# Kernel optimization log

Measured on AMD Instinct MI355X. Metric: run time of the kernel, lower is better.

Reference implementation:

```python
import jax, jax.numpy as jnp
import numpy as np

HIDDEN = 1024
MOE_FF = 512
SHARED_FF = 2816
NUM_EXPERTS = 16
TOP_K = 2
NORM_TOPK = True


def setup_inputs() -> dict:
    key = jax.random.key(0)
    ks = jax.random.split(key, 8)
    s = 0.02
    return {
        "layer_input": jax.random.normal(ks[0], (1, 2048, HIDDEN), dtype=jnp.float32),
        "gate_w": jax.random.normal(ks[1], (NUM_EXPERTS, HIDDEN), dtype=jnp.float32) * s,
        # fused gate_up weight per expert, laid out for x @ W: [E, hidden, 2*moe_ff]
        "w_gate_up": jax.random.normal(ks[2], (NUM_EXPERTS, HIDDEN, 2 * MOE_FF), dtype=jnp.float32) * s,
        # down weight per expert, laid out for h @ W: [E, moe_ff, hidden]
        "w_down": jax.random.normal(ks[3], (NUM_EXPERTS, MOE_FF, HIDDEN), dtype=jnp.float32) * s,
        # shared expert (Qwen2MoeMLP): Linear weights stored torch-style [out, in]
        "shared_w_gate": jax.random.normal(ks[4], (SHARED_FF, HIDDEN), dtype=jnp.float32) * s,
        "shared_w_up": jax.random.normal(ks[5], (SHARED_FF, HIDDEN), dtype=jnp.float32) * s,
        "shared_w_down": jax.random.normal(ks[6], (HIDDEN, SHARED_FF), dtype=jnp.float32) * s,
        "shared_gate_w": jax.random.normal(ks[7], (1, HIDDEN), dtype=jnp.float32) * s,
    }


def reference(layer_input, gate_w, w_gate_up, w_down,
              shared_w_gate, shared_w_up, shared_w_down, shared_gate_w):
    B, S, D = layer_input.shape
    x = layer_input.reshape(-1, D)  # [N, D]
    N = x.shape[0]

    # shared expert: silu-gated MLP, scaled by per-token sigmoid gate
    shared = (jax.nn.silu(x @ shared_w_gate.T) * (x @ shared_w_up.T)) @ shared_w_down.T
    shared = shared * jax.nn.sigmoid(x @ shared_gate_w.T)  # [N, D]

    # router: softmax in float32, top-k, optional renorm
    logits = x @ gate_w.T  # [N, E]
    probs = jax.nn.softmax(logits.astype(jnp.float32), axis=-1)
    rw, sel = jax.lax.top_k(probs, TOP_K)  # [N, K]
    if NORM_TOPK:
        rw = rw / rw.sum(axis=-1, keepdims=True)
    rw = rw.astype(x.dtype)

    # dense combine weights: zero for unselected experts (equivalent to
    # the sort/dispatch + grouped-GEMM + weighted scatter-combine)
    combine = jnp.zeros((N, NUM_EXPERTS), x.dtype).at[jnp.arange(N)[:, None], sel].set(rw)

    # expert gate_up projection, SwiGLU, down projection, weighted combine
    gu = jnp.einsum('nd,edf->nef', x, w_gate_up)  # [N, E, 2*moe_ff]
    g, h = jnp.split(gu, 2, axis=-1)
    h = jax.nn.silu(g) * h  # [N, E, moe_ff]
    expert_out = jnp.einsum('nef,efd,ne->nd', h, w_down, combine)  # [N, D]

    out = expert_out + shared
    return out.reshape(B, S, D)
```

## Files before the change

kernel.cpp:

```cpp
#include <hip/hip_runtime.h>
#include <hip/hip_bf16.h>

typedef unsigned short ushort_t;
typedef __bf16 bf16x8 __attribute__((ext_vector_type(8)));
typedef float f32x4 __attribute__((ext_vector_type(4)));

#define N_TOK 2048
#define DH    1024
#define FF    512
#define SFF   2816
#define NE    16

#define BM 128
#define BN 64
#define BK 64
#define LDK 72

__device__ __forceinline__ ushort_t f2bf(float f) {
  unsigned int x = __float_as_uint(f);
  unsigned int lsb = (x >> 16) & 1u;
  x += 0x7fffu + lsb;
  return (ushort_t)(x >> 16);
}
__device__ __forceinline__ float bf2f(ushort_t u) {
  union { unsigned int i; float f; } v; v.i = ((unsigned int)u) << 16; return v.f;
}
__device__ __forceinline__ uint4 cvt8v(const float4 a, const float4 b) {
  union { ushort_t u[8]; uint4 v; } r;
  r.u[0] = f2bf(a.x); r.u[1] = f2bf(a.y); r.u[2] = f2bf(a.z); r.u[3] = f2bf(a.w);
  r.u[4] = f2bf(b.x); r.u[5] = f2bf(b.y); r.u[6] = f2bf(b.z); r.u[7] = f2bf(b.w);
  return r.v;
}
__device__ __forceinline__ uint4 ld_cvt8(const float* __restrict__ p) {
  float4 a = *(const float4*)p;
  float4 b = *(const float4*)(p + 4);
  return cvt8v(a, b);
}

__global__ void router_kernel(const float* __restrict__ X, const float* __restrict__ GW,
                              const float* __restrict__ SGW,
                              int* __restrict__ sel, float* __restrict__ wtk,
                              float* __restrict__ sgate) {
  int wave = threadIdx.x >> 6, lane = threadIdx.x & 63;
  int n = blockIdx.x * 4 + wave;
  const float* x = X + (size_t)n * DH;
  int e = lane & 15, s = lane >> 4;
  const float* gw = GW + (size_t)e * DH;
  float lg = 0.f;
  for (int i = 0; i < 256; ++i) {
    int d = s * 256 + i;
    lg += x[d] * gw[d];
  }
  lg += __shfl_down(lg, 32);
  lg += __shfl_down(lg, 16);

  float gd = 0.f;
  #pragma unroll
  for (int i = 0; i < 16; ++i) {
    int d = lane * 16 + i;
    gd += x[d] * SGW[d];
  }
  #pragma unroll
  for (int off = 32; off >= 1; off >>= 1) gd += __shfl_down(gd, off);

  float l[16];
  #pragma unroll
  for (int i = 0; i < 16; ++i) l[i] = __shfl(lg, i);

  if (lane == 0) {
    int i1 = 0; float v1 = l[0];
    #pragma unroll
    for (int i = 1; i < 16; ++i) if (l[i] > v1) { v1 = l[i]; i1 = i; }
    int i2 = -1; float v2 = -1e30f;
    #pragma unroll
    for (int i = 0; i < 16; ++i) { if (i == i1) continue; if (l[i] > v2) { v2 = l[i]; i2 = i; } }
    float p2 = __expf(v2 - v1);
    float inv = 1.f / (1.f + p2);
    sel[n * 2 + 0] = i1; sel[n * 2 + 1] = i2;
    wtk[n * 2 + 0] = inv; wtk[n * 2 + 1] = p2 * inv;
    sgate[n] = 1.f / (1.f + __expf(-gd));
  }
}

__global__ void scatter_kernel(const int* __restrict__ sel,
                               int* __restrict__ toks, int* __restrict__ slot_of,
                               int* __restrict__ offs) {
  __shared__ int cnt[NE], bas[NE];
  int t = threadIdx.x;
  if (t < NE) cnt[t] = 0;
  __syncthreads();
  for (int i = t; i < N_TOK * 2; i += 256) atomicAdd(&cnt[sel[i]], 1);
  __syncthreads();
  if (t == 0) {
    int s = 0;
    for (int e = 0; e < NE; ++e) { bas[e] = s; offs[e] = s; s += cnt[e]; }
    offs[NE] = s;
  }
  __syncthreads();
  if (t < NE) cnt[t] = 0;
  __syncthreads();
  for (int i = t; i < N_TOK * 2; i += 256) {
    int e = sel[i];
    int p = atomicAdd(&cnt[e], 1);
    int slot = bas[e] + p;
    toks[slot] = i >> 1;
    slot_of[i] = slot;
  }
}

__global__ __launch_bounds__(256, 3) void gateup_kernel(
    const float* __restrict__ X, const float* __restrict__ WGU,
    const float* __restrict__ SWG, const float* __restrict__ SWU,
    ushort_t* __restrict__ HX, ushort_t* __restrict__ HS,
    const int* __restrict__ toks, const int* __restrict__ offs) {
  __shared__ __align__(16) ushort_t As[BM][LDK];
  __shared__ __align__(16) ushort_t Bgs[BN][LDK];
  __shared__ __align__(16) ushort_t Bus[BN][LDK];
  const int K = DH, NT = K / BK;

  int bid = blockIdx.x;
  int t = threadIdx.x;
  int wave = t >> 6, lane = t & 63;
  int wm = wave & 1, wn = wave >> 1;
  int qd = lane >> 4, l16 = lane & 15;
  int sr = t >> 3, sc = (t & 7) * 8;

  f32x4 accg[4][2], accu[4][2];
  #pragma unroll
  for (int i = 0; i < 4; ++i)
    #pragma unroll
    for (int j = 0; j < 2; ++j) {
      accg[i][j] = (f32x4){0.f, 0.f, 0.f, 0.f};
      accu[i][j] = (f32x4){0.f, 0.f, 0.f, 0.f};
    }

  int m0, n0, M, base, is_exp;

  if (bid < 704) {
    is_exp = 0; base = 0; M = N_TOK;
    n0 = (bid % 44) * BN; m0 = (bid / 44) * BM;
    const float* arow[4];
    const float *bgrow[2], *burow[2];
    #pragma unroll
    for (int p = 0; p < 4; ++p)
      arow[p] = X + (size_t)(m0 + sr + 32 * p) * K + sc;
    #pragma unroll
    for (int p = 0; p < 2; ++p) {
      bgrow[p] = SWG + (size_t)(n0 + sr + 32 * p) * K + sc;
      burow[p] = SWU + (size_t)(n0 + sr + 32 * p) * K + sc;
    }
    uint4 ar[4], bgr[2], bur[2];
    #pragma unroll
    for (int p = 0; p < 4; ++p) ar[p] = ld_cvt8(arow[p]);
    #pragma unroll
    for (int p = 0; p < 2; ++p) { bgr[p] = ld_cvt8(bgrow[p]); bur[p] = ld_cvt8(burow[p]); }

    for (int kt = 0; kt < NT; ++kt) {
      #pragma unroll
      for (int p = 0; p < 4; ++p)
        *(uint4*)&As[sr + 32 * p][sc] = ar[p];
      #pragma unroll
      for (int p = 0; p < 2; ++p) {
        *(uint4*)&Bgs[sr + 32 * p][sc] = bgr[p];
        *(uint4*)&Bus[sr + 32 * p][sc] = bur[p];
      }
      __syncthreads();
      if (kt + 1 < NT) {
        int ko = (kt + 1) * BK;
        #pragma unroll
        for (int p = 0; p < 4; ++p) ar[p] = ld_cvt8(arow[p] + ko);
        #pragma unroll
        for (int p = 0; p < 2; ++p) { bgr[p] = ld_cvt8(bgrow[p] + ko); bur[p] = ld_cvt8(burow[p] + ko); }
      }
      #pragma unroll
      for (int ks = 0; ks < 2; ++ks) {
        int kk = ks * 32 + qd * 8;
        bf16x8 af[4], bgf[2], buf[2];
        #pragma unroll
        for (int i = 0; i < 4; ++i)
          af[i] = *(const bf16x8*)&As[wm * 64 + i * 16 + l16][kk];
        #pragma unroll
        for (int j = 0; j < 2; ++j) {
          bgf[j] = *(const bf16x8*)&Bgs[wn * 32 + j * 16 + l16][kk];
          buf[j] = *(const bf16x8*)&Bus[wn * 32 + j * 16 + l16][kk];
        }
        #pragma unroll
        for (int i = 0; i < 4; ++i)
          #pragma unroll
          for (int j = 0; j < 2; ++j) {
            accg[i][j] = __builtin_amdgcn_mfma_f32_16x16x32_bf16(af[i], bgf[j], accg[i][j], 0, 0, 0);
            accu[i][j] = __builtin_amdgcn_mfma_f32_16x16x32_bf16(af[i], buf[j], accu[i][j], 0, 0, 0);
          }
      }
      __syncthreads();
    }
  } else {
    is_exp = 1;
    int b2 = bid - 704;
    int e = b2 >> 7, rem = b2 & 127;
    n0 = (rem & 7) * BN; m0 = (rem >> 3) * BM;
    base = offs[e]; M = offs[e + 1] - base;
    if (m0 >= M) return;
    const float* W = WGU + (size_t)e * DH * (2 * FF);
    int tn = t & 63, tk = (t >> 6) * 16;

    const float* arow[4];
    #pragma unroll
    for (int p = 0; p < 4; ++p) {
      int m = m0 + sr + 32 * p;
      int mm = m < M ? m : (M - 1);
      arow[p] = X + (size_t)toks[base + mm] * K + sc;
    }
    const float* wkb = W + (size_t)tk * (2 * FF) + n0 + tn;

    uint4 ar[4];
    float bgr[16], bur[16];
    #pragma unroll
    for (int p = 0; p < 4; ++p) ar[p] = ld_cvt8(arow[p]);
    #pragma unroll
    for (int j = 0; j < 16; ++j) {
      bgr[j] = wkb[(size_t)j * (2 * FF)];
      bur[j] = wkb[(size_t)j * (2 * FF) + FF];
    }

    for (int kt = 0; kt < NT; ++kt) {
      #pragma unroll
      for (int p = 0; p < 4; ++p)
        *(uint4*)&As[sr + 32 * p][sc] = ar[p];
      {
        union { ushort_t u[8]; uint4 v; } g0, g1, u0, u1;
        #pragma unroll
        for (int j = 0; j < 8; ++j) {
          g0.u[j] = f2bf(bgr[j]); g1.u[j] = f2bf(bgr[8 + j]);
          u0.u[j] = f2bf(bur[j]); u1.u[j] = f2bf(bur[8 + j]);
        }
        *(uint4*)&Bgs[tn][tk]     = g0.v;
        *(uint4*)&Bgs[tn][tk + 8] = g1.v;
        *(uint4*)&Bus[tn][tk]     = u0.v;
        *(uint4*)&Bus[tn][tk + 8] = u1.v;
      }
      __syncthreads();
      if (kt + 1 < NT) {
        int ko = (kt + 1) * BK;
        #pragma unroll
        for (int p = 0; p < 4; ++p) ar[p] = ld_cvt8(arow[p] + ko);
        const float* wk = wkb + (size_t)ko * (2 * FF);
        #pragma unroll
        for (int j = 0; j < 16; ++j) {
          bgr[j] = wk[(size_t)j * (2 * FF)];
          bur[j] = wk[(size_t)j * (2 * FF) + FF];
        }
      }
      #pragma unroll
      for (int ks = 0; ks < 2; ++ks) {
        int kk = ks * 32 + qd * 8;
        bf16x8 af[4], bgf[2], buf[2];
        #pragma unroll
        for (int i = 0; i < 4; ++i)
          af[i] = *(const bf16x8*)&As[wm * 64 + i * 16 + l16][kk];
        #pragma unroll
        for (int j = 0; j < 2; ++j) {
          bgf[j] = *(const bf16x8*)&Bgs[wn * 32 + j * 16 + l16][kk];
          buf[j] = *(const bf16x8*)&Bus[wn * 32 + j * 16 + l16][kk];
        }
        #pragma unroll
        for (int i = 0; i < 4; ++i)
          #pragma unroll
          for (int j = 0; j < 2; ++j) {
            accg[i][j] = __builtin_amdgcn_mfma_f32_16x16x32_bf16(af[i], bgf[j], accg[i][j], 0, 0, 0);
            accu[i][j] = __builtin_amdgcn_mfma_f32_16x16x32_bf16(af[i], buf[j], accu[i][j], 0, 0, 0);
          }
      }
      __syncthreads();
    }
  }

  #pragma unroll
  for (int i = 0; i < 4; ++i)
    #pragma unroll
    for (int r = 0; r < 4; ++r) {
      int row = wm * 64 + i * 16 + qd * 4 + r;
      #pragma unroll
      for (int j = 0; j < 2; ++j) {
        float g = accg[i][j][r], u = accu[i][j][r];
        float h = g / (1.f + __expf(-g)) * u;
        As[row][wn * 32 + j * 16 + l16] = f2bf(h);
      }
    }
  __syncthreads();
  if (is_exp) {
    #pragma unroll
    for (int p = 0; p < 4; ++p) {
      int m = m0 + sr + 32 * p;
      if (m < M)
        *(uint4*)(HX + (size_t)(base + m) * FF + n0 + sc) = *(uint4*)&As[sr + 32 * p][sc];
    }
  } else {
    #pragma unroll
    for (int p = 0; p < 4; ++p) {
      int m = m0 + sr + 32 * p;
      *(uint4*)(HS + (size_t)m * SFF + n0 + sc) = *(uint4*)&As[sr + 32 * p][sc];
    }
  }
}

__global__ __launch_bounds__(256, 4) void down_kernel(
    const ushort_t* __restrict__ HX, const ushort_t* __restrict__ HS,
    const float* __restrict__ WDN, const float* __restrict__ SWD,
    ushort_t* __restrict__ SD0, ushort_t* __restrict__ SD1,
    ushort_t* __restrict__ EXPO, const int* __restrict__ offs) {
  __shared__ __align__(16) ushort_t As[BM][LDK];
  __shared__ __align__(16) ushort_t Bs[BN][LDK];

  int bid = blockIdx.x;
  int t = threadIdx.x;
  int wave = t >> 6, lane = t & 63;
  int wm = wave & 1, wn = wave >> 1;
  int qd = lane >> 4, l16 = lane & 15;
  int sr = t >> 3, sc = (t & 7) * 8;

  f32x4 c[4][2];
  #pragma unroll
  for (int i = 0; i < 4; ++i)
    #pragma unroll
    for (int j = 0; j < 2; ++j) c[i][j] = (f32x4){0.f, 0.f, 0.f, 0.f};

  int m0, n0, M, base_row;
  ushort_t* outp;

  if (bid < 512) {
    int kz = bid >> 8, rem = bid & 255;
    m0 = (rem >> 4) * BM; n0 = (rem & 15) * BN;
    M = N_TOK; base_row = 0;
    const int KC = SFF / 2, NT = KC / BK;
    int kb = kz * KC;
    outp = kz ? SD1 : SD0;

    const ushort_t* arow[4];
    const float* brow[2];
    #pragma unroll
    for (int p = 0; p < 4; ++p)
      arow[p] = HS + (size_t)(m0 + sr + 32 * p) * SFF + kb + sc;
    #pragma unroll
    for (int p = 0; p < 2; ++p)
      brow[p] = SWD + (size_t)(n0 + sr + 32 * p) * SFF + kb + sc;

    uint4 ar[4], br[2];
    #pragma unroll
    for (int p = 0; p < 4; ++p) ar[p] = *(const uint4*)(arow[p]);
    #pragma unroll
    for (int p = 0; p < 2; ++p) br[p] = ld_cvt8(brow[p]);

    for (int kt = 0; kt < NT; ++kt) {
      #pragma unroll
      for (int p = 0; p < 4; ++p)
        *(uint4*)&As[sr + 32 * p][sc] = ar[p];
      #pragma unroll
      for (int p = 0; p < 2; ++p)
        *(uint4*)&Bs[sr + 32 * p][sc] = br[p];
      __syncthreads();
      if (kt + 1 < NT) {
        int ko = (kt + 1) * BK;
        #pragma unroll
        for (int p = 0; p < 4; ++p) ar[p] = *(const uint4*)(arow[p] + ko);
        #pragma unroll
        for (int p = 0; p < 2; ++p) br[p] = ld_cvt8(brow[p] + ko);
      }
      #pragma unroll
      for (int ks = 0; ks < 2; ++ks) {
        int kk = ks * 32 + qd * 8;
        bf16x8 af[4], bf[2];
        #pragma unroll
        for (int i = 0; i < 4; ++i)
          af[i] = *(const bf16x8*)&As[wm * 64 + i * 16 + l16][kk];
        #pragma unroll
        for (int j = 0; j < 2; ++j)
          bf[j] = *(const bf16x8*)&Bs[wn * 32 + j * 16 + l16][kk];
        #pragma unroll
        for (int i = 0; i < 4; ++i)
          #pragma unroll
          for (int j = 0; j < 2; ++j)
            c[i][j] = __builtin_amdgcn_mfma_f32_16x16x32_bf16(af[i], bf[j], c[i][j], 0, 0, 0);
      }
      __syncthreads();
    }
  } else {
    int b2 = bid - 512;
    int e = b2 >> 8, rem = b2 & 255;
    n0 = (rem & 15) * BN; m0 = (rem >> 4) * BM;
    int base = offs[e];
    M = offs[e + 1] - base;
    if (m0 >= M) return;
    base_row = base;
    const int NT = FF / BK;
    const float* W = WDN + (size_t)e * FF * DH;
    const ushort_t* A = HX + (size_t)base * FF;
    int tn = t & 63, tk = (t >> 6) * 16;
    outp = EXPO;

    const ushort_t* arow[4];
    #pragma unroll
    for (int p = 0; p < 4; ++p) {
      int m = m0 + sr + 32 * p;
      int mm = m < M ? m : (M - 1);
      arow[p] = A + (size_t)mm * FF + sc;
    }
    const float* wkb = W + (size_t)tk * DH + n0 + tn;

    uint4 ar[4];
    float br[16];
    #pragma unroll
    for (int p = 0; p < 4; ++p) ar[p] = *(const uint4*)(arow[p]);
    #pragma unroll
    for (int j = 0; j < 16; ++j) br[j] = wkb[(size_t)j * DH];

    for (int kt = 0; kt < NT; ++kt) {
      #pragma unroll
      for (int p = 0; p < 4; ++p)
        *(uint4*)&As[sr + 32 * p][sc] = ar[p];
      {
        union { ushort_t u[8]; uint4 v; } b0, b1;
        #pragma unroll
        for (int j = 0; j < 8; ++j) { b0.u[j] = f2bf(br[j]); b1.u[j] = f2bf(br[8 + j]); }
        *(uint4*)&Bs[tn][tk]     = b0.v;
        *(uint4*)&Bs[tn][tk + 8] = b1.v;
      }
      __syncthreads();
      if (kt + 1 < NT) {
        int ko = (kt + 1) * BK;
        #pragma unroll
        for (int p = 0; p < 4; ++p) ar[p] = *(const uint4*)(arow[p] + ko);
        const float* wk = wkb + (size_t)ko * DH;
        #pragma unroll
        for (int j = 0; j < 16; ++j) br[j] = wk[(size_t)j * DH];
      }
      #pragma unroll
      for (int ks = 0; ks < 2; ++ks) {
        int kk = ks * 32 + qd * 8;
        bf16x8 af[4], bf[2];
        #pragma unroll
        for (int i = 0; i < 4; ++i)
          af[i] = *(const bf16x8*)&As[wm * 64 + i * 16 + l16][kk];
        #pragma unroll
        for (int j = 0; j < 2; ++j)
          bf[j] = *(const bf16x8*)&Bs[wn * 32 + j * 16 + l16][kk];
        #pragma unroll
        for (int i = 0; i < 4; ++i)
          #pragma unroll
          for (int j = 0; j < 2; ++j)
            c[i][j] = __builtin_amdgcn_mfma_f32_16x16x32_bf16(af[i], bf[j], c[i][j], 0, 0, 0);
      }
      __syncthreads();
    }
  }

  #pragma unroll
  for (int i = 0; i < 4; ++i)
    #pragma unroll
    for (int r = 0; r < 4; ++r) {
      int row = wm * 64 + i * 16 + qd * 4 + r;
      #pragma unroll
      for (int j = 0; j < 2; ++j)
        As[row][wn * 32 + j * 16 + l16] = f2bf(c[i][j][r]);
    }
  __syncthreads();
  #pragma unroll
  for (int p = 0; p < 4; ++p) {
    int m = m0 + sr + 32 * p;
    if (m < M)
      *(uint4*)(outp + (size_t)(base_row + m) * DH + n0 + sc) = *(uint4*)&As[sr + 32 * p][sc];
  }
}

__global__ void combine_kernel(const ushort_t* __restrict__ SD0, const ushort_t* __restrict__ SD1,
                               const ushort_t* __restrict__ EXPO,
                               const float* __restrict__ sgate, const float* __restrict__ wtk,
                               const int* __restrict__ slot_of, float* __restrict__ out) {
  int n = blockIdx.x, t = threadIdx.x;
  float sg = sgate[n];
  float w0 = wtk[n * 2 + 0], w1 = wtk[n * 2 + 1];
  int s0 = slot_of[n * 2 + 0], s1 = slot_of[n * 2 + 1];
  int col = t * 4;
  ushort4 d0 = *(const ushort4*)(SD0 + (size_t)n * DH + col);
  ushort4 d1 = *(const ushort4*)(SD1 + (size_t)n * DH + col);
  ushort4 a  = *(const ushort4*)(EXPO + (size_t)s0 * DH + col);
  ushort4 b  = *(const ushort4*)(EXPO + (size_t)s1 * DH + col);
  float4 o;
  o.x = sg * (bf2f(d0.x) + bf2f(d1.x)) + w0 * bf2f(a.x) + w1 * bf2f(b.x);
  o.y = sg * (bf2f(d0.y) + bf2f(d1.y)) + w0 * bf2f(a.y) + w1 * bf2f(b.y);
  o.z = sg * (bf2f(d0.z) + bf2f(d1.z)) + w0 * bf2f(a.z) + w1 * bf2f(b.z);
  o.w = sg * (bf2f(d0.w) + bf2f(d1.w)) + w0 * bf2f(a.w) + w1 * bf2f(b.w);
  *(float4*)(out + (size_t)n * DH + col) = o;
}

extern "C" void kernel_launch(void* const* d_in, const int* in_sizes, int n_in,
                              void* d_out, int out_size, void* d_ws, size_t ws_size,
                              hipStream_t stream) {
  const float* x    = (const float*)d_in[0];
  const float* gw   = (const float*)d_in[1];
  const float* wgu  = (const float*)d_in[2];
  const float* wdn  = (const float*)d_in[3];
  const float* swg  = (const float*)d_in[4];
  const float* swu  = (const float*)d_in[5];
  const float* swd  = (const float*)d_in[6];
  const float* sgw  = (const float*)d_in[7];
  float* out = (float*)d_out;

  char* ws = (char*)d_ws;
  constexpr size_t OFF_HS   = 0;
  constexpr size_t OFF_HX   = OFF_HS   + (size_t)N_TOK * SFF * 2;
  constexpr size_t OFF_SD0  = OFF_HX   + (size_t)4096 * FF * 2;
  constexpr size_t OFF_SD1  = OFF_SD0  + (size_t)N_TOK * DH * 2;
  constexpr size_t OFF_EXPO = OFF_SD1  + (size_t)N_TOK * DH * 2;
  constexpr size_t OFF_TOK  = OFF_EXPO + (size_t)4096 * DH * 2;
  constexpr size_t OFF_OFFS = OFF_TOK  + 4096 * 4;
  constexpr size_t OFF_SEL  = OFF_OFFS + 32 * 4;
  constexpr size_t OFF_WTK  = OFF_SEL  + 4096 * 4;
  constexpr size_t OFF_SG   = OFF_WTK  + 4096 * 4;
  constexpr size_t OFF_SLOT = OFF_SG   + 2048 * 4;

  ushort_t* hs    = (ushort_t*)(ws + OFF_HS);
  ushort_t* hx    = (ushort_t*)(ws + OFF_HX);
  ushort_t* sd0   = (ushort_t*)(ws + OFF_SD0);
  ushort_t* sd1   = (ushort_t*)(ws + OFF_SD1);
  ushort_t* expo  = (ushort_t*)(ws + OFF_EXPO);
  int*      toks  = (int*)(ws + OFF_TOK);
  int*      offs  = (int*)(ws + OFF_OFFS);
  int*      sel   = (int*)(ws + OFF_SEL);
  float*    wtk   = (float*)(ws + OFF_WTK);
  float*    sgate = (float*)(ws + OFF_SG);
  int*      slot_of = (int*)(ws + OFF_SLOT);

  router_kernel<<<N_TOK / 4, 256, 0, stream>>>(x, gw, sgw, sel, wtk, sgate);
  scatter_kernel<<<1, 256, 0, stream>>>(sel, toks, slot_of, offs);
  gateup_kernel<<<704 + 2048, 256, 0, stream>>>(x, wgu, swg, swu, hx, hs, toks, offs);
  down_kernel<<<512 + 4096, 256, 0, stream>>>(hx, hs, wdn, swd, sd0, sd1, expo, offs);
  combine_kernel<<<N_TOK, 256, 0, stream>>>(sd0, sd1, expo, sgate, wtk, slot_of, out);
}
```

Baseline: 409.4 us.

## Pre-convert activations and shared weights to bf16 in a separate kernel

Adds a convert kernel that casts the input activations and the three shared-expert weight matrices from fp32 to bf16 once per call. The gate-up and down GEMMs then load bf16 directly instead of loading fp32 and converting per tile. This halves the global traffic inside those GEMMs and drops the repeated conversion work, at the cost of an extra kernel that reads all the fp32 data and writes the bf16 copies. It also switches f2bf to the native __bf16 cast and raises the launch-bounds occupancy hints on both GEMM kernels.

```diff
diff --git a/kernel.cpp b/kernel.cpp
--- a/kernel.cpp
+++ b/kernel.cpp
@@ -17,10 +17,8 @@
 #define LDK 72
 
 __device__ __forceinline__ ushort_t f2bf(float f) {
-  unsigned int x = __float_as_uint(f);
-  unsigned int lsb = (x >> 16) & 1u;
-  x += 0x7fffu + lsb;
-  return (ushort_t)(x >> 16);
+  __bf16 h = (__bf16)f;
+  union { __bf16 h; ushort_t u; } v; v.h = h; return v.u;
 }
 __device__ __forceinline__ float bf2f(ushort_t u) {
   union { unsigned int i; float f; } v; v.i = ((unsigned int)u) << 16; return v.f;
@@ -35,6 +33,21 @@
   float4 a = *(const float4*)p;
   float4 b = *(const float4*)(p + 4);
   return cvt8v(a, b);
+}
+
+__global__ void convert_kernel(const float* __restrict__ X, const float* __restrict__ SWG,
+                               const float* __restrict__ SWU, const float* __restrict__ SWD,
+                               ushort_t* __restrict__ XB, ushort_t* __restrict__ SWGB,
+                               ushort_t* __restrict__ SWUB, ushort_t* __restrict__ SWDB) {
+  const int NX = N_TOK * DH / 8;
+  const int NS = SFF * DH / 8;
+  int i = blockIdx.x * 256 + threadIdx.x;
+  const float* s; ushort_t* d; int off;
+  if (i < NX)               { s = X;   d = XB;   off = i; }
+  else if (i < NX + NS)     { s = SWG; d = SWGB; off = i - NX; }
+  else if (i < NX + 2 * NS) { s = SWU; d = SWUB; off = i - NX - NS; }
+  else                      { s = SWD; d = SWDB; off = i - NX - 2 * NS; }
+  *(uint4*)(d + (size_t)off * 8) = ld_cvt8(s + (size_t)off * 8);
 }
 
 __global__ void router_kernel(const float* __restrict__ X, const float* __restrict__ GW,
@@ -108,9 +121,9 @@
   }
 }
 
-__global__ __launch_bounds__(256, 3) void gateup_kernel(
-    const float* __restrict__ X, const float* __restrict__ WGU,
-    const float* __restrict__ SWG, const float* __restrict__ SWU,
+__global__ __launch_bounds__(256, 4) void gateup_kernel(
+    const ushort_t* __restrict__ XB, const float* __restrict__ WGU,
+    const ushort_t* __restrict__ SWGB, const ushort_t* __restrict__ SWUB,
     ushort_t* __restrict__ HX, ushort_t* __restrict__ HS,
     const int* __restrict__ toks, const int* __restrict__ offs) {
   __shared__ __align__(16) ushort_t As[BM][LDK];
@@ -139,21 +152,21 @@
   if (bid < 704) {
     is_exp = 0; base = 0; M = N_TOK;
     n0 = (bid % 44) * BN; m0 = (bid / 44) * BM;
-    const float* arow[4];
-    const float *bgrow[2], *burow[2];
+    const ushort_t* arow[4];
+    const ushort_t *bgrow[2], *burow[2];
     #pragma unroll
     for (int p = 0; p < 4; ++p)
-      arow[p] = X + (size_t)(m0 + sr + 32 * p) * K + sc;
+      arow[p] = XB + (size_t)(m0 + sr + 32 * p) * K + sc;
     #pragma unroll
     for (int p = 0; p < 2; ++p) {
-      bgrow[p] = SWG + (size_t)(n0 + sr + 32 * p) * K + sc;
-      burow[p] = SWU + (size_t)(n0 + sr + 32 * p) * K + sc;
+      bgrow[p] = SWGB + (size_t)(n0 + sr + 32 * p) * K + sc;
+      burow[p] = SWUB + (size_t)(n0 + sr + 32 * p) * K + sc;
     }
     uint4 ar[4], bgr[2], bur[2];
     #pragma unroll
-    for (int p = 0; p < 4; ++p) ar[p] = ld_cvt8(arow[p]);
-    #pragma unroll
-    for (int p = 0; p < 2; ++p) { bgr[p] = ld_cvt8(bgrow[p]); bur[p] = ld_cvt8(burow[p]); }
+    for (int p = 0; p < 4; ++p) ar[p] = *(const uint4*)arow[p];
+    #pragma unroll
+    for (int p = 0; p < 2; ++p) { bgr[p] = *(const uint4*)bgrow[p]; bur[p] = *(const uint4*)burow[p]; }
 
     for (int kt = 0; kt < NT; ++kt) {
       #pragma unroll
@@ -168,9 +181,9 @@
       if (kt + 1 < NT) {
         int ko = (kt + 1) * BK;
         #pragma unroll
-        for (int p = 0; p < 4; ++p) ar[p] = ld_cvt8(arow[p] + ko);
-        #pragma unroll
-        for (int p = 0; p < 2; ++p) { bgr[p] = ld_cvt8(bgrow[p] + ko); bur[p] = ld_cvt8(burow[p] + ko); }
+        for (int p = 0; p < 4; ++p) ar[p] = *(const uint4*)(arow[p] + ko);
+        #pragma unroll
+        for (int p = 0; p < 2; ++p) { bgr[p] = *(const uint4*)(bgrow[p] + ko); bur[p] = *(const uint4*)(burow[p] + ko); }
       }
       #pragma unroll
       for (int ks = 0; ks < 2; ++ks) {
@@ -204,19 +217,19 @@
     const float* W = WGU + (size_t)e * DH * (2 * FF);
     int tn = t & 63, tk = (t >> 6) * 16;
 
-    const float* arow[4];
+    const ushort_t* arow[4];
     #pragma unroll
     for (int p = 0; p < 4; ++p) {
       int m = m0 + sr + 32 * p;
       int mm = m < M ? m : (M - 1);
-      arow[p] = X + (size_t)toks[base + mm] * K + sc;
+      arow[p] = XB + (size_t)toks[base + mm] * K + sc;
     }
     const float* wkb = W + (size_t)tk * (2 * FF) + n0 + tn;
 
     uint4 ar[4];
     float bgr[16], bur[16];
     #pragma unroll
-    for (int p = 0; p < 4; ++p) ar[p] = ld_cvt8(arow[p]);
+    for (int p = 0; p < 4; ++p) ar[p] = *(const uint4*)arow[p];
     #pragma unroll
     for (int j = 0; j < 16; ++j) {
       bgr[j] = wkb[(size_t)j * (2 * FF)];
@@ -243,7 +256,7 @@
       if (kt + 1 < NT) {
         int ko = (kt + 1) * BK;
         #pragma unroll
-        for (int p = 0; p < 4; ++p) ar[p] = ld_cvt8(arow[p] + ko);
+        for (int p = 0; p < 4; ++p) ar[p] = *(const uint4*)(arow[p] + ko);
         const float* wk = wkb + (size_t)ko * (2 * FF);
         #pragma unroll
         for (int j = 0; j < 16; ++j) {
@@ -304,9 +317,9 @@
   }
 }
 
-__global__ __launch_bounds__(256, 4) void down_kernel(
+__global__ __launch_bounds__(256, 5) void down_kernel(
     const ushort_t* __restrict__ HX, const ushort_t* __restrict__ HS,
-    const float* __restrict__ WDN, const float* __restrict__ SWD,
+    const float* __restrict__ WDN, const ushort_t* __restrict__ SWDB,
     ushort_t* __restrict__ SD0, ushort_t* __restrict__ SD1,
     ushort_t* __restrict__ EXPO, const int* __restrict__ offs) {
   __shared__ __align__(16) ushort_t As[BM][LDK];
@@ -337,19 +350,19 @@
     outp = kz ? SD1 : SD0;
 
     const ushort_t* arow[4];
-    const float* brow[2];
+    const ushort_t* brow[2];
     #pragma unroll
     for (int p = 0; p < 4; ++p)
       arow[p] = HS + (size_t)(m0 + sr + 32 * p) * SFF + kb + sc;
     #pragma unroll
     for (int p = 0; p < 2; ++p)
-      brow[p] = SWD + (size_t)(n0 + sr + 32 * p) * SFF + kb + sc;
+      brow[p] = SWDB + (size_t)(n0 + sr + 32 * p) * SFF + kb + sc;
 
     uint4 ar[4], br[2];
     #pragma unroll
     for (int p = 0; p < 4; ++p) ar[p] = *(const uint4*)(arow[p]);
     #pragma unroll
-    for (int p = 0; p < 2; ++p) br[p] = ld_cvt8(brow[p]);
+    for (int p = 0; p < 2; ++p) br[p] = *(const uint4*)(brow[p]);
 
     for (int kt = 0; kt < NT; ++kt) {
       #pragma unroll
@@ -364,7 +377,7 @@
         #pragma unroll
         for (int p = 0; p < 4; ++p) ar[p] = *(const uint4*)(arow[p] + ko);
         #pragma unroll
-        for (int p = 0; p < 2; ++p) br[p] = ld_cvt8(brow[p] + ko);
+        for (int p = 0; p < 2; ++p) br[p] = *(const uint4*)(brow[p] + ko);
       }
       #pragma unroll
       for (int ks = 0; ks < 2; ++ks) {
@@ -512,7 +525,11 @@
   constexpr size_t OFF_SD0  = OFF_HX   + (size_t)4096 * FF * 2;
   constexpr size_t OFF_SD1  = OFF_SD0  + (size_t)N_TOK * DH * 2;
   constexpr size_t OFF_EXPO = OFF_SD1  + (size_t)N_TOK * DH * 2;
-  constexpr size_t OFF_TOK  = OFF_EXPO + (size_t)4096 * DH * 2;
+  constexpr size_t OFF_XB   = OFF_EXPO + (size_t)4096 * DH * 2;
+  constexpr size_t OFF_SWGB = OFF_XB   + (size_t)N_TOK * DH * 2;
+  constexpr size_t OFF_SWUB = OFF_SWGB + (size_t)SFF * DH * 2;
+  constexpr size_t OFF_SWDB = OFF_SWUB + (size_t)SFF * DH * 2;
+  constexpr size_t OFF_TOK  = OFF_SWDB + (size_t)SFF * DH * 2;
   constexpr size_t OFF_OFFS = OFF_TOK  + 4096 * 4;
   constexpr size_t OFF_SEL  = OFF_OFFS + 32 * 4;
   constexpr size_t OFF_WTK  = OFF_SEL  + 4096 * 4;
@@ -524,6 +541,10 @@
   ushort_t* sd0   = (ushort_t*)(ws + OFF_SD0);
   ushort_t* sd1   = (ushort_t*)(ws + OFF_SD1);
   ushort_t* expo  = (ushort_t*)(ws + OFF_EXPO);
+  ushort_t* xb    = (ushort_t*)(ws + OFF_XB);
+  ushort_t* swgb  = (ushort_t*)(ws + OFF_SWGB);
+  ushort_t* swub  = (ushort_t*)(ws + OFF_SWUB);
+  ushort_t* swdb  = (ushort_t*)(ws + OFF_SWDB);
   int*      toks  = (int*)(ws + OFF_TOK);
   int*      offs  = (int*)(ws + OFF_OFFS);
   int*      sel   = (int*)(ws + OFF_SEL);
@@ -531,9 +552,10 @@
   float*    sgate = (float*)(ws + OFF_SG);
   int*      slot_of = (int*)(ws + OFF_SLOT);
 
+  convert_kernel<<<5248, 256, 0, stream>>>(x, swg, swu, swd, xb, swgb, swub, swdb);
   router_kernel<<<N_TOK / 4, 256, 0, stream>>>(x, gw, sgw, sel, wtk, sgate);
   scatter_kernel<<<1, 256, 0, stream>>>(sel, toks, slot_of, offs);
-  gateup_kernel<<<704 + 2048, 256, 0, stream>>>(x, wgu, swg, swu, hx, hs, toks, offs);
-  down_kernel<<<512 + 4096, 256, 0, stream>>>(hx, hs, wdn, swd, sd0, sd1, expo, offs);
+  gateup_kernel<<<704 + 2048, 256, 0, stream>>>(xb, wgu, swgb, swub, hx, hs, toks, offs);
+  down_kernel<<<512 + 4096, 256, 0, stream>>>(hx, hs, wdn, swdb, sd0, sd1, expo, offs);
   combine_kernel<<<N_TOK, 256, 0, stream>>>(sd0, sd1, expo, sgate, wtk, slot_of, out);
 }
```

After: 514.7 us. 25.7% more time.

## Pre-transpose and bf16-convert expert weights into K-contiguous workspace layout

Applied to the files above, without the earlier changes.

Adds a per-call kernel that transposes and converts the fp32 expert gate_up and down weights into bf16 [N][K] layout in workspace. The expert GEMM paths then load B tiles with 16-byte vector loads and store them straight into shared memory, with no per-element conversion. This replaces the old scattered strided scalar fp32 weight loads. The cost is an extra pass that reads all expert weights (about 96MB fp32) and writes them back as bf16, run on every call.

```diff
diff --git a/kernel.cpp b/kernel.cpp
--- a/kernel.cpp
+++ b/kernel.cpp
@@ -35,6 +35,39 @@
   float4 a = *(const float4*)p;
   float4 b = *(const float4*)(p + 4);
   return cvt8v(a, b);
+}
+
+__global__ void transpose_kernel(const float* __restrict__ WGU, const float* __restrict__ WDN,
+                                 ushort_t* __restrict__ WGUB, ushort_t* __restrict__ WDNB) {
+  __shared__ ushort_t tl[64][72];
+  int bid = blockIdx.x;
+  const float* src; ushort_t* dst; int K, N, kt, nt;
+  if (bid < 4096) {
+    int e = bid >> 8, rem = bid & 255; kt = rem >> 4; nt = rem & 15;
+    src = WGU + (size_t)e * DH * (2 * FF); dst = WGUB + (size_t)e * (2 * FF) * DH;
+    K = DH; N = 2 * FF;
+  } else {
+    int b2 = bid - 4096;
+    int e = b2 >> 7, rem = b2 & 127; kt = rem >> 4; nt = rem & 15;
+    src = WDN + (size_t)e * FF * DH; dst = WDNB + (size_t)e * DH * FF;
+    K = FF; N = DH;
+  }
+  int t = threadIdx.x;
+  int k0 = kt * 64, n0 = nt * 64;
+  int r = t >> 2, c0 = (t & 3) * 16;
+  const float* sp = src + (size_t)(k0 + r) * N + n0 + c0;
+  #pragma unroll
+  for (int q = 0; q < 4; ++q) {
+    float4 v = *(const float4*)(sp + q * 4);
+    tl[c0 + q * 4 + 0][r] = f2bf(v.x);
+    tl[c0 + q * 4 + 1][r] = f2bf(v.y);
+    tl[c0 + q * 4 + 2][r] = f2bf(v.z);
+    tl[c0 + q * 4 + 3][r] = f2bf(v.w);
+  }
+  __syncthreads();
+  ushort_t* dp = dst + (size_t)(n0 + r) * K + k0 + c0;
+  *(uint4*)(dp)     = *(uint4*)&tl[r][c0];
+  *(uint4*)(dp + 8) = *(uint4*)&tl[r][c0 + 8];
 }
 
 __global__ void router_kernel(const float* __restrict__ X, const float* __restrict__ GW,
@@ -109,7 +142,7 @@
 }
 
 __global__ __launch_bounds__(256, 3) void gateup_kernel(
-    const float* __restrict__ X, const float* __restrict__ WGU,
+    const float* __restrict__ X, const ushort_t* __restrict__ WGUB,
     const float* __restrict__ SWG, const float* __restrict__ SWU,
     ushort_t* __restrict__ HX, ushort_t* __restrict__ HS,
     const int* __restrict__ toks, const int* __restrict__ offs) {
@@ -201,8 +234,7 @@
     n0 = (rem & 7) * BN; m0 = (rem >> 3) * BM;
     base = offs[e]; M = offs[e + 1] - base;
     if (m0 >= M) return;
-    const float* W = WGU + (size_t)e * DH * (2 * FF);
-    int tn = t & 63, tk = (t >> 6) * 16;
+    const ushort_t* Wt = WGUB + (size_t)e * (2 * FF) * DH;
 
     const float* arow[4];
     #pragma unroll
@@ -211,45 +243,35 @@
       int mm = m < M ? m : (M - 1);
       arow[p] = X + (size_t)toks[base + mm] * K + sc;
     }
-    const float* wkb = W + (size_t)tk * (2 * FF) + n0 + tn;
-
-    uint4 ar[4];
-    float bgr[16], bur[16];
+    const ushort_t *bgrow[2], *burow[2];
+    #pragma unroll
+    for (int p = 0; p < 2; ++p) {
+      bgrow[p] = Wt + (size_t)(n0 + sr + 32 * p) * DH + sc;
+      burow[p] = Wt + (size_t)(FF + n0 + sr + 32 * p) * DH + sc;
+    }
+
+    uint4 ar[4], bgr[2], bur[2];
     #pragma unroll
     for (int p = 0; p < 4; ++p) ar[p] = ld_cvt8(arow[p]);
     #pragma unroll
-    for (int j = 0; j < 16; ++j) {
-      bgr[j] = wkb[(size_t)j * (2 * FF)];
-      bur[j] = wkb[(size_t)j * (2 * FF) + FF];
-    }
+    for (int p = 0; p < 2; ++p) { bgr[p] = *(const uint4*)bgrow[p]; bur[p] = *(const uint4*)burow[p]; }
 
     for (int kt = 0; kt < NT; ++kt) {
       #pragma unroll
       for (int p = 0; p < 4; ++p)
         *(uint4*)&As[sr + 32 * p][sc] = ar[p];
-      {
-        union { ushort_t u[8]; uint4 v; } g0, g1, u0, u1;
-        #pragma unroll
-        for (int j = 0; j < 8; ++j) {
-          g0.u[j] = f2bf(bgr[j]); g1.u[j] = f2bf(bgr[8 + j]);
-          u0.u[j] = f2bf(bur[j]); u1.u[j] = f2bf(bur[8 + j]);
-        }
-        *(uint4*)&Bgs[tn][tk]     = g0.v;
-        *(uint4*)&Bgs[tn][tk + 8] = g1.v;
-        *(uint4*)&Bus[tn][tk]     = u0.v;
-        *(uint4*)&Bus[tn][tk + 8] = u1.v;
+      #pragma unroll
+      for (int p = 0; p < 2; ++p) {
+        *(uint4*)&Bgs[sr + 32 * p][sc] = bgr[p];
+        *(uint4*)&Bus[sr + 32 * p][sc] = bur[p];
       }
       __syncthreads();
       if (kt + 1 < NT) {
         int ko = (kt + 1) * BK;
         #pragma unroll
         for (int p = 0; p < 4; ++p) ar[p] = ld_cvt8(arow[p] + ko);
-        const float* wk = wkb + (size_t)ko * (2 * FF);
-        #pragma unroll
-        for (int j = 0; j < 16; ++j) {
-          bgr[j] = wk[(size_t)j * (2 * FF)];
-          bur[j] = wk[(size_t)j * (2 * FF) + FF];
-        }
+        #pragma unroll
+        for (int p = 0; p < 2; ++p) { bgr[p] = *(const uint4*)(bgrow[p] + ko); bur[p] = *(const uint4*)(burow[p] + ko); }
       }
       #pragma unroll
       for (int ks = 0; ks < 2; ++ks) {
@@ -306,7 +328,7 @@
 
 __global__ __launch_bounds__(256, 4) void down_kernel(
     const ushort_t* __restrict__ HX, const ushort_t* __restrict__ HS,
-    const float* __restrict__ WDN, const float* __restrict__ SWD,
+    const ushort_t* __restrict__ WDNB, const float* __restrict__ SWD,
     ushort_t* __restrict__ SD0, ushort_t* __restrict__ SD1,
     ushort_t* __restrict__ EXPO, const int* __restrict__ offs) {
   __shared__ __align__(16) ushort_t As[BM][LDK];
@@ -393,9 +415,8 @@
     if (m0 >= M) return;
     base_row = base;
     const int NT = FF / BK;
-    const float* W = WDN + (size_t)e * FF * DH;
+    const ushort_t* Wd = WDNB + (size_t)e * DH * FF;
     const ushort_t* A = HX + (size_t)base * FF;
-    int tn = t & 63, tk = (t >> 6) * 16;
     outp = EXPO;
 
     const ushort_t* arow[4];
@@ -405,34 +426,31 @@
       int mm = m < M ? m : (M - 1);
       arow[p] = A + (size_t)mm * FF + sc;
     }
-    const float* wkb = W + (size_t)tk * DH + n0 + tn;
-
-    uint4 ar[4];
-    float br[16];
+    const ushort_t* brow[2];
+    #pragma unroll
+    for (int p = 0; p < 2; ++p)
+      brow[p] = Wd + (size_t)(n0 + sr + 32 * p) * FF + sc;
+
+    uint4 ar[4], br[2];
     #pragma unroll
     for (int p = 0; p < 4; ++p) ar[p] = *(const uint4*)(arow[p]);
     #pragma unroll
-    for (int j = 0; j < 16; ++j) br[j] = wkb[(size_t)j * DH];
+    for (int p = 0; p < 2; ++p) br[p] = *(const uint4*)(brow[p]);
 
     for (int kt = 0; kt < NT; ++kt) {
       #pragma unroll
       for (int p = 0; p < 4; ++p)
         *(uint4*)&As[sr + 32 * p][sc] = ar[p];
-      {
-        union { ushort_t u[8]; uint4 v; } b0, b1;
-        #pragma unroll
-        for (int j = 0; j < 8; ++j) { b0.u[j] = f2bf(br[j]); b1.u[j] = f2bf(br[8 + j]); }
-        *(uint4*)&Bs[tn][tk]     = b0.v;
-        *(uint4*)&Bs[tn][tk + 8] = b1.v;
-      }
+      #pragma unroll
+      for (int p = 0; p < 2; ++p)
+        *(uint4*)&Bs[sr + 32 * p][sc] = br[p];
       __syncthreads();
       if (kt + 1 < NT) {
         int ko = (kt + 1) * BK;
         #pragma unroll
         for (int p = 0; p < 4; ++p) ar[p] = *(const uint4*)(arow[p] + ko);
-        const float* wk = wkb + (size_t)ko * DH;
-        #pragma unroll
-        for (int j = 0; j < 16; ++j) br[j] = wk[(size_t)j * DH];
+        #pragma unroll
+        for (int p = 0; p < 2; ++p) br[p] = *(const uint4*)(brow[p] + ko);
       }
       #pragma unroll
       for (int ks = 0; ks < 2; ++ks) {
@@ -512,7 +530,9 @@
   constexpr size_t OFF_SD0  = OFF_HX   + (size_t)4096 * FF * 2;
   constexpr size_t OFF_SD1  = OFF_SD0  + (size_t)N_TOK * DH * 2;
   constexpr size_t OFF_EXPO = OFF_SD1  + (size_t)N_TOK * DH * 2;
-  constexpr size_t OFF_TOK  = OFF_EXPO + (size_t)4096 * DH * 2;
+  constexpr size_t OFF_WGUB = OFF_EXPO + (size_t)4096 * DH * 2;
+  constexpr size_t OFF_WDNB = OFF_WGUB + (size_t)NE * (2 * FF) * DH * 2;
+  constexpr size_t OFF_TOK  = OFF_WDNB + (size_t)NE * DH * FF * 2;
   constexpr size_t OFF_OFFS = OFF_TOK  + 4096 * 4;
   constexpr size_t OFF_SEL  = OFF_OFFS + 32 * 4;
   constexpr size_t OFF_WTK  = OFF_SEL  + 4096 * 4;
@@ -524,6 +544,8 @@
   ushort_t* sd0   = (ushort_t*)(ws + OFF_SD0);
   ushort_t* sd1   = (ushort_t*)(ws + OFF_SD1);
   ushort_t* expo  = (ushort_t*)(ws + OFF_EXPO);
+  ushort_t* wgub  = (ushort_t*)(ws + OFF_WGUB);
+  ushort_t* wdnb  = (ushort_t*)(ws + OFF_WDNB);
   int*      toks  = (int*)(ws + OFF_TOK);
   int*      offs  = (int*)(ws + OFF_OFFS);
   int*      sel   = (int*)(ws + OFF_SEL);
@@ -531,9 +553,10 @@
   float*    sgate = (float*)(ws + OFF_SG);
   int*      slot_of = (int*)(ws + OFF_SLOT);
 
+  transpose_kernel<<<4096 + 2048, 256, 0, stream>>>(wgu, wdn, wgub, wdnb);
   router_kernel<<<N_TOK / 4, 256, 0, stream>>>(x, gw, sgw, sel, wtk, sgate);
   scatter_kernel<<<1, 256, 0, stream>>>(sel, toks, slot_of, offs);
-  gateup_kernel<<<704 + 2048, 256, 0, stream>>>(x, wgu, swg, swu, hx, hs, toks, offs);
-  down_kernel<<<512 + 4096, 256, 0, stream>>>(hx, hs, wdn, swd, sd0, sd1, expo, offs);
+  gateup_kernel<<<704 + 2048, 256, 0, stream>>>(x, wgub, swg, swu, hx, hs, toks, offs);
+  down_kernel<<<512 + 4096, 256, 0, stream>>>(hx, hs, wdnb, swd, sd0, sd1, expo, offs);
   combine_kernel<<<N_TOK, 256, 0, stream>>>(sd0, sd1, expo, sgate, wtk, slot_of, out);
 }
```

After: 460.1 us. +12.4%, slower.

## Pre-transpose expert down weights to bf16 and vectorize router dot products

Applied to the files above, without the earlier changes.

Adds a kernel that converts the expert down-projection weights to bf16 and transposes them to [E, hidden, ff], so down_kernel can load B tiles with contiguous 16-byte reads instead of strided scalar fp32 loads followed by per-element conversion. The router's logit and shared-gate dot products also switch to float4 loads. The transpose runs on every call, costing an extra 32 MB fp32 read and 16 MB bf16 write, while the many down_kernel tiles that reread each expert's weights become cheaper.

```diff
diff --git a/kernel.cpp b/kernel.cpp
--- a/kernel.cpp
+++ b/kernel.cpp
@@ -35,6 +35,31 @@
   float4 a = *(const float4*)p;
   float4 b = *(const float4*)(p + 4);
   return cvt8v(a, b);
+}
+
+__global__ void transpose_kernel(const float* __restrict__ WDN, ushort_t* __restrict__ WDNB) {
+  __shared__ ushort_t tl[64][72];
+  int bid = blockIdx.x;
+  int e = bid >> 7, rem = bid & 127;
+  int kt = rem >> 4, nt = rem & 15;
+  const float* src = WDN + (size_t)e * FF * DH;
+  ushort_t* dst = WDNB + (size_t)e * DH * FF;
+  int t = threadIdx.x;
+  int k0 = kt * 64, n0 = nt * 64;
+  int r = t >> 2, c0 = (t & 3) * 16;
+  const float* sp = src + (size_t)(k0 + r) * DH + n0 + c0;
+  #pragma unroll
+  for (int q = 0; q < 4; ++q) {
+    float4 v = *(const float4*)(sp + q * 4);
+    tl[c0 + q * 4 + 0][r] = f2bf(v.x);
+    tl[c0 + q * 4 + 1][r] = f2bf(v.y);
+    tl[c0 + q * 4 + 2][r] = f2bf(v.z);
+    tl[c0 + q * 4 + 3][r] = f2bf(v.w);
+  }
+  __syncthreads();
+  ushort_t* dp = dst + (size_t)(n0 + r) * FF + k0 + c0;
+  *(uint4*)(dp)     = *(uint4*)&tl[r][c0];
+  *(uint4*)(dp + 8) = *(uint4*)&tl[r][c0 + 8];
 }
 
 __global__ void router_kernel(const float* __restrict__ X, const float* __restrict__ GW,
@@ -47,18 +72,23 @@
   int e = lane & 15, s = lane >> 4;
   const float* gw = GW + (size_t)e * DH;
   float lg = 0.f;
-  for (int i = 0; i < 256; ++i) {
-    int d = s * 256 + i;
-    lg += x[d] * gw[d];
+  #pragma unroll
+  for (int i = 0; i < 64; ++i) {
+    int d = s * 256 + i * 4;
+    float4 xv = *(const float4*)(x + d);
+    float4 gv = *(const float4*)(gw + d);
+    lg += xv.x * gv.x + xv.y * gv.y + xv.z * gv.z + xv.w * gv.w;
   }
   lg += __shfl_down(lg, 32);
   lg += __shfl_down(lg, 16);
 
   float gd = 0.f;
   #pragma unroll
-  for (int i = 0; i < 16; ++i) {
-    int d = lane * 16 + i;
-    gd += x[d] * SGW[d];
+  for (int i = 0; i < 4; ++i) {
+    int d = lane * 16 + i * 4;
+    float4 xv = *(const float4*)(x + d);
+    float4 gv = *(const float4*)(SGW + d);
+    gd += xv.x * gv.x + xv.y * gv.y + xv.z * gv.z + xv.w * gv.w;
   }
   #pragma unroll
   for (int off = 32; off >= 1; off >>= 1) gd += __shfl_down(gd, off);
@@ -306,7 +336,7 @@
 
 __global__ __launch_bounds__(256, 4) void down_kernel(
     const ushort_t* __restrict__ HX, const ushort_t* __restrict__ HS,
-    const float* __restrict__ WDN, const float* __restrict__ SWD,
+    const ushort_t* __restrict__ WDNB, const float* __restrict__ SWD,
     ushort_t* __restrict__ SD0, ushort_t* __restrict__ SD1,
     ushort_t* __restrict__ EXPO, const int* __restrict__ offs) {
   __shared__ __align__(16) ushort_t As[BM][LDK];
@@ -393,9 +423,8 @@
     if (m0 >= M) return;
     base_row = base;
     const int NT = FF / BK;
-    const float* W = WDN + (size_t)e * FF * DH;
+    const ushort_t* Wd = WDNB + (size_t)e * DH * FF;
     const ushort_t* A = HX + (size_t)base * FF;
-    int tn = t & 63, tk = (t >> 6) * 16;
     outp = EXPO;
 
     const ushort_t* arow[4];
@@ -405,34 +434,31 @@
       int mm = m < M ? m : (M - 1);
       arow[p] = A + (size_t)mm * FF + sc;
     }
-    const float* wkb = W + (size_t)tk * DH + n0 + tn;
-
-    uint4 ar[4];
-    float br[16];
+    const ushort_t* brow[2];
+    #pragma unroll
+    for (int p = 0; p < 2; ++p)
+      brow[p] = Wd + (size_t)(n0 + sr + 32 * p) * FF + sc;
+
+    uint4 ar[4], br[2];
     #pragma unroll
     for (int p = 0; p < 4; ++p) ar[p] = *(const uint4*)(arow[p]);
     #pragma unroll
-    for (int j = 0; j < 16; ++j) br[j] = wkb[(size_t)j * DH];
+    for (int p = 0; p < 2; ++p) br[p] = *(const uint4*)(brow[p]);
 
     for (int kt = 0; kt < NT; ++kt) {
       #pragma unroll
       for (int p = 0; p < 4; ++p)
         *(uint4*)&As[sr + 32 * p][sc] = ar[p];
-      {
-        union { ushort_t u[8]; uint4 v; } b0, b1;
-        #pragma unroll
-        for (int j = 0; j < 8; ++j) { b0.u[j] = f2bf(br[j]); b1.u[j] = f2bf(br[8 + j]); }
-        *(uint4*)&Bs[tn][tk]     = b0.v;
-        *(uint4*)&Bs[tn][tk + 8] = b1.v;
-      }
+      #pragma unroll
+      for (int p = 0; p < 2; ++p)
+        *(uint4*)&Bs[sr + 32 * p][sc] = br[p];
       __syncthreads();
       if (kt + 1 < NT) {
         int ko = (kt + 1) * BK;
         #pragma unroll
         for (int p = 0; p < 4; ++p) ar[p] = *(const uint4*)(arow[p] + ko);
-        const float* wk = wkb + (size_t)ko * DH;
-        #pragma unroll
-        for (int j = 0; j < 16; ++j) br[j] = wk[(size_t)j * DH];
+        #pragma unroll
+        for (int p = 0; p < 2; ++p) br[p] = *(const uint4*)(brow[p] + ko);
       }
       #pragma unroll
       for (int ks = 0; ks < 2; ++ks) {
@@ -512,7 +538,8 @@
   constexpr size_t OFF_SD0  = OFF_HX   + (size_t)4096 * FF * 2;
   constexpr size_t OFF_SD1  = OFF_SD0  + (size_t)N_TOK * DH * 2;
   constexpr size_t OFF_EXPO = OFF_SD1  + (size_t)N_TOK * DH * 2;
-  constexpr size_t OFF_TOK  = OFF_EXPO + (size_t)4096 * DH * 2;
+  constexpr size_t OFF_WDNB = OFF_EXPO + (size_t)4096 * DH * 2;
+  constexpr size_t OFF_TOK  = OFF_WDNB + (size_t)NE * DH * FF * 2;
   constexpr size_t OFF_OFFS = OFF_TOK  + 4096 * 4;
   constexpr size_t OFF_SEL  = OFF_OFFS + 32 * 4;
   constexpr size_t OFF_WTK  = OFF_SEL  + 4096 * 4;
@@ -524,6 +551,7 @@
   ushort_t* sd0   = (ushort_t*)(ws + OFF_SD0);
   ushort_t* sd1   = (ushort_t*)(ws + OFF_SD1);
   ushort_t* expo  = (ushort_t*)(ws + OFF_EXPO);
+  ushort_t* wdnb  = (ushort_t*)(ws + OFF_WDNB);
   int*      toks  = (int*)(ws + OFF_TOK);
   int*      offs  = (int*)(ws + OFF_OFFS);
   int*      sel   = (int*)(ws + OFF_SEL);
@@ -531,9 +559,10 @@
   float*    sgate = (float*)(ws + OFF_SG);
   int*      slot_of = (int*)(ws + OFF_SLOT);
 
+  transpose_kernel<<<2048, 256, 0, stream>>>(wdn, wdnb);
   router_kernel<<<N_TOK / 4, 256, 0, stream>>>(x, gw, sgw, sel, wtk, sgate);
   scatter_kernel<<<1, 256, 0, stream>>>(sel, toks, slot_of, offs);
   gateup_kernel<<<704 + 2048, 256, 0, stream>>>(x, wgu, swg, swu, hx, hs, toks, offs);
-  down_kernel<<<512 + 4096, 256, 0, stream>>>(hx, hs, wdn, swd, sd0, sd1, expo, offs);
+  down_kernel<<<512 + 4096, 256, 0, stream>>>(hx, hs, wdnb, swd, sd0, sd1, expo, offs);
   combine_kernel<<<N_TOK, 256, 0, stream>>>(sd0, sd1, expo, sgate, wtk, slot_of, out);
 }
```

Result: slower. 424.1 us (+3.6%).
